# Performance work log

Measured on AMD Instinct MI355X. Metric: run time of the kernel, lower is better.

The kernel has to match this reference:

```python
import jax, jax.numpy as jnp
import numpy as np

EPS = 1e-5  # torch LayerNorm default


def _layernorm(x, g, b):
    mu = jnp.mean(x, axis=-1, keepdims=True)
    var = jnp.mean(jnp.square(x - mu), axis=-1, keepdims=True)
    return (x - mu) * jax.lax.rsqrt(var + EPS) * g + b


def _sparse_window_attn(x, wq, wk, wv, wo, span, stride, head_num):
    B, L, D = x.shape
    d = D // head_num  # dim_QK == dim_V == dim_q // head_num
    Q = (x @ wq.T).reshape(B, L, head_num, d).transpose(0, 2, 1, 3)  # [B,H,L,d]
    K = (x @ wk.T).reshape(B, L, head_num, d).transpose(0, 2, 1, 3)
    V = (x @ wv.T).reshape(B, L, head_num, d).transpose(0, 2, 1, 3)
    s = jnp.arange(span)
    i = jnp.arange(L)
    kvi = s[:, None] - (span - 1) + stride * i[None, :]       # [S,L] key index per (offset, query)
    valid = (kvi >= 0) & (kvi < L)
    kvic = jnp.clip(kvi, 0, L - 1)
    Kg = K[:, :, kvic, :]                                     # [B,H,S,L,d]
    scores = jnp.einsum('bhld,bhsld->bhsl', Q, Kg) / jnp.sqrt(jnp.float32(d))
    scores = jnp.where(valid[None, None], scores, -jnp.inf)
    p = jax.nn.softmax(scores, axis=2)                        # softmax over span (dim 2 in torch)
    Vg = V[:, :, kvic, :]                                     # [B,H,S,L,d]
    o = jnp.einsum('bhsl,bhsld->bhld', p, Vg)                 # invalid entries have p==0
    o = o.transpose(0, 2, 1, 3).reshape(B, L, D)
    return o @ wo.T


def setup_inputs() -> dict:
    key = jax.random.key(0)
    ks = jax.random.split(key, 8)
    B, L, D = 2, 2048, 512
    sc = 1.0 / np.sqrt(D)
    return {
        'query': jax.random.normal(ks[0], (B, L, D), jnp.float32),
        'ln_g': jnp.ones((D,), jnp.float32),
        'ln_b': jnp.zeros((D,), jnp.float32),
        'wq': jax.random.normal(ks[1], (D, D), jnp.float32) * sc,
        'wk': jax.random.normal(ks[2], (D, D), jnp.float32) * sc,
        'wv': jax.random.normal(ks[3], (D, D), jnp.float32) * sc,
        'wo': jax.random.normal(ks[4], (D, D), jnp.float32) * sc,
        'w1': jax.random.normal(ks[5], (2 * D, D), jnp.float32) * sc,
        'b1': jnp.zeros((2 * D,), jnp.float32),
        'w2': jax.random.normal(ks[6], (D, 2 * D), jnp.float32) * (1.0 / np.sqrt(2 * D)),
        'b2': jnp.zeros((D,), jnp.float32),
        'span': 64,
        'stride': 1,
        'head_num': 8,
    }


def reference(query, ln_g, ln_b, wq, wk, wv, wo, w1, b1, w2, b2, span, stride, head_num):
    # NOTE: the torch block applies the SAME LayerNorm (shared params) twice.
    x = _layernorm(query, ln_g, ln_b)
    x = _sparse_window_attn(x, wq, wk, wv, wo, span, stride, head_num)
    query = x + query
    x = _layernorm(query, ln_g, ln_b)
    x = jax.nn.gelu(x @ w1.T + b1, approximate=False) @ w2.T + b2
    return x + query
```

## Files before the change

### kernel.cpp

```cpp
#include <hip/hip_runtime.h>
#include <hip/hip_bf16.h>
#include <cmath>

typedef __bf16 bf16;
typedef __attribute__((ext_vector_type(8))) __bf16 bf16x8;
typedef __attribute__((ext_vector_type(4))) __bf16 bf16x4;
typedef __attribute__((ext_vector_type(4))) float f32x4;
typedef __attribute__((ext_vector_type(4))) unsigned int u32x4;

#define LD_B 2
#define LD_L 2048
#define LD_D 512
#define N_HEAD 8
#define HD 64
#define NTOK (LD_B * LD_L)
#define QKV_LD 1536

__device__ __forceinline__ void gload16(const void* g, void* l) {
  __builtin_amdgcn_global_load_lds(
      (const __attribute__((address_space(1))) void*)g,
      (__attribute__((address_space(3))) void*)l, 16, 0, 0);
}

__global__ __launch_bounds__(256) void prep_kernel(
    const float* __restrict__ x, const float* __restrict__ g,
    const float* __restrict__ b, bf16* __restrict__ xln,
    const float* __restrict__ s0, const float* __restrict__ s1,
    const float* __restrict__ s2, const float* __restrict__ s3,
    const float* __restrict__ s4, const float* __restrict__ s5,
    bf16* __restrict__ d0, bf16* __restrict__ d1, bf16* __restrict__ d2,
    bf16* __restrict__ d3, bf16* __restrict__ d4, bf16* __restrict__ d5)
{
  if (blockIdx.x >= 1024) {
    int idx = (blockIdx.x - 1024) * 256 + threadIdx.x;
    const float* src; bf16* dst; int off;
    if (idx < 262144) {
      int seg = idx >> 16; off = idx & 65535;
      src = seg == 0 ? s0 : seg == 1 ? s1 : seg == 2 ? s2 : s3;
      dst = seg == 0 ? d0 : seg == 1 ? d1 : seg == 2 ? d2 : d3;
    } else {
      int t = idx - 262144;
      int seg = t >> 17; off = t & 131071;
      src = seg ? s5 : s4;
      dst = seg ? d5 : d4;
    }
    f32x4 v = ((const f32x4*)src)[off];
    bf16x4 o;
    o[0] = (bf16)v[0]; o[1] = (bf16)v[1]; o[2] = (bf16)v[2]; o[3] = (bf16)v[3];
    ((bf16x4*)dst)[off] = o;
    return;
  }
  const int wid = threadIdx.x >> 6, lane = threadIdx.x & 63;
  const int row = blockIdx.x * 4 + wid;
  const f32x4* xr = (const f32x4*)(x + (size_t)row * LD_D);
  f32x4 v0 = xr[lane * 2], v1 = xr[lane * 2 + 1];
  float s = v0[0] + v0[1] + v0[2] + v0[3] + v1[0] + v1[1] + v1[2] + v1[3];
#pragma unroll
  for (int off = 32; off; off >>= 1) s += __shfl_xor(s, off);
  const float mu = s * (1.f / 512.f);
  float vs = 0.f;
#pragma unroll
  for (int i = 0; i < 4; ++i) {
    float a0 = v0[i] - mu; vs += a0 * a0;
    float a1 = v1[i] - mu; vs += a1 * a1;
  }
#pragma unroll
  for (int off = 32; off; off >>= 1) vs += __shfl_xor(vs, off);
  const float rstd = rsqrtf(vs * (1.f / 512.f) + 1e-5f);
  const f32x4* gr = (const f32x4*)g;
  const f32x4* br = (const f32x4*)b;
  f32x4 g0 = gr[lane * 2], g1 = gr[lane * 2 + 1];
  f32x4 b0 = br[lane * 2], b1 = br[lane * 2 + 1];
  bf16x8 o;
#pragma unroll
  for (int i = 0; i < 4; ++i) o[i] = (bf16)((v0[i] - mu) * rstd * g0[i] + b0[i]);
#pragma unroll
  for (int i = 0; i < 4; ++i) o[i + 4] = (bf16)((v1[i] - mu) * rstd * g1[i] + b1[i]);
  *(bf16x8*)(&xln[(size_t)row * LD_D + lane * 8]) = o;
}

__global__ __launch_bounds__(256) void ln_kernel(
    const float* __restrict__ x, const float* __restrict__ g,
    const float* __restrict__ b, bf16* __restrict__ out)
{
  const int wid = threadIdx.x >> 6, lane = threadIdx.x & 63;
  const int row = blockIdx.x * 4 + wid;
  const f32x4* xr = (const f32x4*)(x + (size_t)row * LD_D);
  f32x4 v0 = xr[lane * 2], v1 = xr[lane * 2 + 1];
  float s = v0[0] + v0[1] + v0[2] + v0[3] + v1[0] + v1[1] + v1[2] + v1[3];
#pragma unroll
  for (int off = 32; off; off >>= 1) s += __shfl_xor(s, off);
  const float mu = s * (1.f / 512.f);
  float vs = 0.f;
#pragma unroll
  for (int i = 0; i < 4; ++i) {
    float a0 = v0[i] - mu; vs += a0 * a0;
    float a1 = v1[i] - mu; vs += a1 * a1;
  }
#pragma unroll
  for (int off = 32; off; off >>= 1) vs += __shfl_xor(vs, off);
  const float rstd = rsqrtf(vs * (1.f / 512.f) + 1e-5f);
  const f32x4* gr = (const f32x4*)g;
  const f32x4* br = (const f32x4*)b;
  f32x4 g0 = gr[lane * 2], g1 = gr[lane * 2 + 1];
  f32x4 b0 = br[lane * 2], b1 = br[lane * 2 + 1];
  bf16x8 o;
#pragma unroll
  for (int i = 0; i < 4; ++i) o[i] = (bf16)((v0[i] - mu) * rstd * g0[i] + b0[i]);
#pragma unroll
  for (int i = 0; i < 4; ++i) o[i + 4] = (bf16)((v1[i] - mu) * rstd * g1[i] + b1[i]);
  *(bf16x8*)(&out[(size_t)row * LD_D + lane * 8]) = o;
}

template <int EPI>
__global__ __launch_bounds__(256) void gemm_kernel(
    const bf16* __restrict__ A, const bf16* __restrict__ Bw,
    int M, int N, int K, bf16* __restrict__ Cb, float* __restrict__ Cf,
    const float* __restrict__ bias, const float* __restrict__ res)
{
  __shared__ bf16 As[2][4096];
  __shared__ bf16 Bs[2][4096];
  const int tid = threadIdx.x;
  const int lane = tid & 63, wid = tid >> 6;
  const int wm = wid >> 1, wn = wid & 1;
  const int l15 = lane & 15, kg = lane >> 4;
  const int row0 = blockIdx.x * 64, col0 = blockIdx.y * 64;

  int srow[2], scol[2];
#pragma unroll
  for (int i = 0; i < 2; ++i) {
    int c = i * 256 + tid;
    srow[i] = c >> 3;
    scol[i] = ((c & 7) ^ (srow[i] & 7)) * 8;
  }

  f32x4 acc[2][2];
#pragma unroll
  for (int m = 0; m < 2; ++m)
#pragma unroll
    for (int n = 0; n < 2; ++n) acc[m][n] = (f32x4){0.f, 0.f, 0.f, 0.f};

  const int nt = K >> 6;
#define STAGE(buf, k0)                                                      \
  {                                                                         \
    _Pragma("unroll")                                                       \
    for (int i = 0; i < 2; ++i) {                                           \
      const bf16* ga = A + (size_t)(row0 + srow[i]) * K + (k0) + scol[i];   \
      const bf16* gb = Bw + (size_t)(col0 + srow[i]) * K + (k0) + scol[i];  \
      char* la = (char*)&As[buf][0] + (i * 4 + wid) * 1024;                 \
      char* lb = (char*)&Bs[buf][0] + (i * 4 + wid) * 1024;                 \
      gload16(ga, la);                                                      \
      gload16(gb, lb);                                                      \
    }                                                                       \
  }

  STAGE(0, 0);
  __syncthreads();
  for (int t = 0; t < nt; ++t) {
    if (t + 1 < nt) STAGE((t + 1) & 1, (t + 1) << 6);
    const char* pa = (const char*)&As[t & 1][0];
    const char* pb = (const char*)&Bs[t & 1][0];
#pragma unroll
    for (int kk = 0; kk < 2; ++kk) {
      bf16x8 af[2], bf[2];
#pragma unroll
      for (int m = 0; m < 2; ++m) {
        const int r = wm * 32 + m * 16 + l15;
        int off = r * 128 + kk * 64 + kg * 16;
        off ^= (r & 7) << 4;
        af[m] = *(const bf16x8*)(pa + off);
      }
#pragma unroll
      for (int n = 0; n < 2; ++n) {
        const int r = wn * 32 + n * 16 + l15;
        int off = r * 128 + kk * 64 + kg * 16;
        off ^= (r & 7) << 4;
        bf[n] = *(const bf16x8*)(pb + off);
      }
#pragma unroll
      for (int m = 0; m < 2; ++m)
#pragma unroll
        for (int n = 0; n < 2; ++n)
          acc[m][n] = __builtin_amdgcn_mfma_f32_16x16x32_bf16(af[m], bf[n], acc[m][n], 0, 0, 0);
    }
    __syncthreads();
  }
#undef STAGE

  const int orow = row0 + wm * 32, ocol = col0 + wn * 32;
#pragma unroll
  for (int m = 0; m < 2; ++m) {
#pragma unroll
    for (int n = 0; n < 2; ++n) {
#pragma unroll
      for (int e = 0; e < 4; ++e) {
        const int rr = orow + m * 16 + kg * 4 + e;
        const int cc = ocol + n * 16 + l15;
        const float v = acc[m][n][e];
        const size_t oi = (size_t)rr * N + cc;
        if constexpr (EPI == 0) {
          Cb[oi] = (bf16)v;
        } else if constexpr (EPI == 1) {
          Cf[oi] = v + res[oi];
        } else if constexpr (EPI == 2) {
          float t2 = v + bias[cc];
          Cb[oi] = (bf16)(0.5f * t2 * (1.f + erff(t2 * 0.70710678118654752f)));
        } else {
          Cf[oi] = v + bias[cc] + res[oi];
        }
      }
    }
  }
}

__global__ __launch_bounds__(256) void attn_kernel(
    const bf16* __restrict__ QKV, bf16* __restrict__ Og)
{
  constexpr int STK = 72;
  constexpr int STP = 136;
  __shared__ bf16 Ks[128][STK];
  __shared__ bf16 Qs[64][STK];
  __shared__ bf16 Vt[64][STP];
  __shared__ bf16 Ps[4][16][STP];
  const int tid = threadIdx.x;
  const int qt = blockIdx.x, bh = blockIdx.y;
  const int b = bh >> 3, h = bh & 7;
  const int q0 = qt * 64;
  const int j0 = q0 - 63;
  const size_t baseQ = (size_t)b * LD_L * QKV_LD + h * HD;
  const size_t baseK = baseQ + 512;
  const size_t baseV = baseQ + 1024;
  const size_t baseO = (size_t)b * LD_L * LD_D + h * HD;

  for (int c = tid; c < 128 * 8; c += 256) {
    const int r = c >> 3, d0 = (c & 7) * 8;
    const int j = j0 + r;
    u32x4 kv = (u32x4){0u, 0u, 0u, 0u};
    bf16x8 vv = (bf16x8)(__bf16)0.f;
    if (j >= 0 && j < LD_L) {
      kv = *(const u32x4*)(QKV + baseK + (size_t)j * QKV_LD + d0);
      vv = *(const bf16x8*)(QKV + baseV + (size_t)j * QKV_LD + d0);
    }
    *(u32x4*)(&Ks[r][d0]) = kv;
#pragma unroll
    for (int dd = 0; dd < 8; ++dd) Vt[d0 + dd][r] = vv[dd];
  }
  for (int c = tid; c < 64 * 8; c += 256) {
    const int r = c >> 3, d0 = (c & 7) * 8;
    *(u32x4*)(&Qs[r][d0]) =
        *(const u32x4*)(QKV + baseQ + (size_t)(q0 + r) * QKV_LD + d0);
  }
  __syncthreads();

  const int lane = tid & 63, wid = tid >> 6;
  const int l15 = lane & 15, kg = lane >> 4;
  const int klo = 63 - q0;

  bf16x8 qf[2];
#pragma unroll
  for (int kk = 0; kk < 2; ++kk)
    qf[kk] = *(const bf16x8*)(&Qs[wid * 16 + l15][kk * 32 + kg * 8]);
  f32x4 s[8];
#pragma unroll
  for (int n = 0; n < 8; ++n) s[n] = (f32x4){0.f, 0.f, 0.f, 0.f};
#pragma unroll
  for (int kk = 0; kk < 2; ++kk)
#pragma unroll
    for (int n = 0; n < 8; ++n) {
      bf16x8 kf = *(const bf16x8*)(&Ks[n * 16 + l15][kk * 32 + kg * 8]);
      s[n] = __builtin_amdgcn_mfma_f32_16x16x32_bf16(qf[kk], kf, s[n], 0, 0, 0);
    }

  float p[8][4];
  float mx[4], sm[4];
#pragma unroll
  for (int e = 0; e < 4; ++e) { mx[e] = -INFINITY; sm[e] = 0.f; }
#pragma unroll
  for (int n = 0; n < 8; ++n) {
    const int k = n * 16 + l15;
#pragma unroll
    for (int e = 0; e < 4; ++e) {
      const int qi = wid * 16 + kg * 4 + e;
      const bool ok = (k >= qi) & (k <= qi + 63) & (k >= klo);
      float sv = ok ? s[n][e] * 0.125f : -INFINITY;
      p[n][e] = sv;
      mx[e] = fmaxf(mx[e], sv);
    }
  }
#pragma unroll
  for (int off = 8; off; off >>= 1)
#pragma unroll
    for (int e = 0; e < 4; ++e) mx[e] = fmaxf(mx[e], __shfl_xor(mx[e], off));
#pragma unroll
  for (int n = 0; n < 8; ++n)
#pragma unroll
    for (int e = 0; e < 4; ++e) {
      float pv = (p[n][e] == -INFINITY) ? 0.f : __expf(p[n][e] - mx[e]);
      p[n][e] = pv;
      sm[e] += pv;
    }
#pragma unroll
  for (int off = 8; off; off >>= 1)
#pragma unroll
    for (int e = 0; e < 4; ++e) sm[e] += __shfl_xor(sm[e], off);
  float rs[4];
#pragma unroll
  for (int e = 0; e < 4; ++e) rs[e] = 1.f / sm[e];

#pragma unroll
  for (int n = 0; n < 8; ++n)
#pragma unroll
    for (int e = 0; e < 4; ++e)
      Ps[wid][kg * 4 + e][n * 16 + l15] = (bf16)(p[n][e] * rs[e]);

  f32x4 o[4];
#pragma unroll
  for (int n = 0; n < 4; ++n) o[n] = (f32x4){0.f, 0.f, 0.f, 0.f};
#pragma unroll
  for (int ks = 0; ks < 4; ++ks) {
    bf16x8 pf = *(const bf16x8*)(&Ps[wid][l15][ks * 32 + kg * 8]);
#pragma unroll
    for (int n = 0; n < 4; ++n) {
      bf16x8 vf = *(const bf16x8*)(&Vt[n * 16 + l15][ks * 32 + kg * 8]);
      o[n] = __builtin_amdgcn_mfma_f32_16x16x32_bf16(pf, vf, o[n], 0, 0, 0);
    }
  }

  const int q = q0 + wid * 16 + kg * 4;
#pragma unroll
  for (int n = 0; n < 4; ++n)
#pragma unroll
    for (int e = 0; e < 4; ++e)
      Og[baseO + (size_t)(q + e) * LD_D + n * 16 + l15] = (bf16)o[n][e];
}

extern "C" void kernel_launch(void* const* d_in, const int* in_sizes, int n_in,
                              void* d_out, int out_size, void* d_ws, size_t ws_size,
                              hipStream_t stream)
{
  const float* query = (const float*)d_in[0];
  const float* ln_g = (const float*)d_in[1];
  const float* ln_b = (const float*)d_in[2];
  const float* wq = (const float*)d_in[3];
  const float* wk = (const float*)d_in[4];
  const float* wv = (const float*)d_in[5];
  const float* wo = (const float*)d_in[6];
  const float* w1 = (const float*)d_in[7];
  const float* b1 = (const float*)d_in[8];
  const float* w2 = (const float*)d_in[9];
  const float* b2 = (const float*)d_in[10];
  float* out = (float*)d_out;

  char* ws = (char*)d_ws;
  bf16* WQKVb = (bf16*)(ws + 0x000000);
  bf16* WOb = (bf16*)(ws + 0x180000);
  bf16* W1b = (bf16*)(ws + 0x200000);
  bf16* W2b = (bf16*)(ws + 0x300000);
  bf16* XLN = (bf16*)(ws + 0x400000);
  bf16* QKVb = (bf16*)(ws + 0x800000);
  bf16* ATb = (bf16*)(ws + 0x1400000);
  float* Q2 = (float*)(ws + 0x1800000);
  bf16* YLN = (bf16*)(ws + 0x2000000);
  bf16* Hb = (bf16*)(ws + 0x2400000);

  prep_kernel<<<3072, 256, 0, stream>>>(
      query, ln_g, ln_b, XLN,
      wq, wk, wv, wo, w1, w2,
      WQKVb, WQKVb + 262144, WQKVb + 524288, WOb, W1b, W2b);
  gemm_kernel<0><<<dim3(64, 24), 256, 0, stream>>>(
      XLN, WQKVb, NTOK, QKV_LD, 512, QKVb, nullptr, nullptr, nullptr);
  attn_kernel<<<dim3(32, 16), 256, 0, stream>>>(QKVb, ATb);
  gemm_kernel<1><<<dim3(64, 8), 256, 0, stream>>>(
      ATb, WOb, NTOK, 512, 512, nullptr, Q2, nullptr, query);
  ln_kernel<<<1024, 256, 0, stream>>>(Q2, ln_g, ln_b, YLN);
  gemm_kernel<2><<<dim3(64, 16), 256, 0, stream>>>(
      YLN, W1b, NTOK, 1024, 512, Hb, nullptr, b1, nullptr);
  gemm_kernel<3><<<dim3(64, 8), 256, 0, stream>>>(
      Hb, W2b, NTOK, 512, 1024, nullptr, out, b2, Q2);
}
```

Before: 149.8 us.

## Fuse all stages into one persistent cooperative kernel with grid syncs

Replaces the seven separate kernel launches (prep, QKV GEMM, attention, out-proj GEMM, LN, FFN1, FFN2) with a single persistent cooperative kernel. Each stage loops over tiles with a grid-stride loop, and stages are separated by grid.sync(). Shared memory is now one shared byte buffer carved up per stage. This removes launch gaps and per-kernel tail effects. In exchange it caps the grid at 512 blocks, adds grid-wide barrier costs, and limits occupancy, since all stages must share one register and LDS budget.

```diff
diff --git a/kernel.cpp b/kernel.cpp
--- a/kernel.cpp
+++ b/kernel.cpp
@@ -1,6 +1,9 @@
 #include <hip/hip_runtime.h>
 #include <hip/hip_bf16.h>
+#include <hip/hip_cooperative_groups.h>
 #include <cmath>
+
+namespace cg = cooperative_groups;
 
 typedef __bf16 bf16;
 typedef __attribute__((ext_vector_type(8))) __bf16 bf16x8;
@@ -11,10 +14,11 @@
 #define LD_B 2
 #define LD_L 2048
 #define LD_D 512
-#define N_HEAD 8
 #define HD 64
 #define NTOK (LD_B * LD_L)
 #define QKV_LD 1536
+
+#define SMEM_BYTES 62464
 
 __device__ __forceinline__ void gload16(const void* g, void* l) {
   __builtin_amdgcn_global_load_lds(
@@ -22,36 +26,10 @@
       (__attribute__((address_space(3))) void*)l, 16, 0, 0);
 }
 
-__global__ __launch_bounds__(256) void prep_kernel(
+__device__ __forceinline__ void ln_row(
     const float* __restrict__ x, const float* __restrict__ g,
-    const float* __restrict__ b, bf16* __restrict__ xln,
-    const float* __restrict__ s0, const float* __restrict__ s1,
-    const float* __restrict__ s2, const float* __restrict__ s3,
-    const float* __restrict__ s4, const float* __restrict__ s5,
-    bf16* __restrict__ d0, bf16* __restrict__ d1, bf16* __restrict__ d2,
-    bf16* __restrict__ d3, bf16* __restrict__ d4, bf16* __restrict__ d5)
-{
-  if (blockIdx.x >= 1024) {
-    int idx = (blockIdx.x - 1024) * 256 + threadIdx.x;
-    const float* src; bf16* dst; int off;
-    if (idx < 262144) {
-      int seg = idx >> 16; off = idx & 65535;
-      src = seg == 0 ? s0 : seg == 1 ? s1 : seg == 2 ? s2 : s3;
-      dst = seg == 0 ? d0 : seg == 1 ? d1 : seg == 2 ? d2 : d3;
-    } else {
-      int t = idx - 262144;
-      int seg = t >> 17; off = t & 131071;
-      src = seg ? s5 : s4;
-      dst = seg ? d5 : d4;
-    }
-    f32x4 v = ((const f32x4*)src)[off];
-    bf16x4 o;
-    o[0] = (bf16)v[0]; o[1] = (bf16)v[1]; o[2] = (bf16)v[2]; o[3] = (bf16)v[3];
-    ((bf16x4*)dst)[off] = o;
-    return;
-  }
-  const int wid = threadIdx.x >> 6, lane = threadIdx.x & 63;
-  const int row = blockIdx.x * 4 + wid;
+    const float* __restrict__ b, bf16* __restrict__ out, int row, int lane)
+{
   const f32x4* xr = (const f32x4*)(x + (size_t)row * LD_D);
   f32x4 v0 = xr[lane * 2], v1 = xr[lane * 2 + 1];
   float s = v0[0] + v0[1] + v0[2] + v0[3] + v1[0] + v1[1] + v1[2] + v1[3];
@@ -76,63 +54,24 @@
   for (int i = 0; i < 4; ++i) o[i] = (bf16)((v0[i] - mu) * rstd * g0[i] + b0[i]);
 #pragma unroll
   for (int i = 0; i < 4; ++i) o[i + 4] = (bf16)((v1[i] - mu) * rstd * g1[i] + b1[i]);
-  *(bf16x8*)(&xln[(size_t)row * LD_D + lane * 8]) = o;
-}
-
-__global__ __launch_bounds__(256) void ln_kernel(
-    const float* __restrict__ x, const float* __restrict__ g,
-    const float* __restrict__ b, bf16* __restrict__ out)
-{
-  const int wid = threadIdx.x >> 6, lane = threadIdx.x & 63;
-  const int row = blockIdx.x * 4 + wid;
-  const f32x4* xr = (const f32x4*)(x + (size_t)row * LD_D);
-  f32x4 v0 = xr[lane * 2], v1 = xr[lane * 2 + 1];
-  float s = v0[0] + v0[1] + v0[2] + v0[3] + v1[0] + v1[1] + v1[2] + v1[3];
-#pragma unroll
-  for (int off = 32; off; off >>= 1) s += __shfl_xor(s, off);
-  const float mu = s * (1.f / 512.f);
-  float vs = 0.f;
-#pragma unroll
-  for (int i = 0; i < 4; ++i) {
-    float a0 = v0[i] - mu; vs += a0 * a0;
-    float a1 = v1[i] - mu; vs += a1 * a1;
-  }
-#pragma unroll
-  for (int off = 32; off; off >>= 1) vs += __shfl_xor(vs, off);
-  const float rstd = rsqrtf(vs * (1.f / 512.f) + 1e-5f);
-  const f32x4* gr = (const f32x4*)g;
-  const f32x4* br = (const f32x4*)b;
-  f32x4 g0 = gr[lane * 2], g1 = gr[lane * 2 + 1];
-  f32x4 b0 = br[lane * 2], b1 = br[lane * 2 + 1];
-  bf16x8 o;
-#pragma unroll
-  for (int i = 0; i < 4; ++i) o[i] = (bf16)((v0[i] - mu) * rstd * g0[i] + b0[i]);
-#pragma unroll
-  for (int i = 0; i < 4; ++i) o[i + 4] = (bf16)((v1[i] - mu) * rstd * g1[i] + b1[i]);
   *(bf16x8*)(&out[(size_t)row * LD_D + lane * 8]) = o;
 }
 
 template <int EPI>
-__global__ __launch_bounds__(256) void gemm_kernel(
+__device__ __forceinline__ void gemm_tile(
     const bf16* __restrict__ A, const bf16* __restrict__ Bw,
-    int M, int N, int K, bf16* __restrict__ Cb, float* __restrict__ Cf,
-    const float* __restrict__ bias, const float* __restrict__ res)
-{
-  __shared__ bf16 As[2][4096];
-  __shared__ bf16 Bs[2][4096];
+    int N, int K, bf16* __restrict__ Cb, float* __restrict__ Cf,
+    const float* __restrict__ bias, const float* __restrict__ res,
+    int row0, int col0, char* __restrict__ smem)
+{
   const int tid = threadIdx.x;
   const int lane = tid & 63, wid = tid >> 6;
   const int wm = wid >> 1, wn = wid & 1;
   const int l15 = lane & 15, kg = lane >> 4;
-  const int row0 = blockIdx.x * 64, col0 = blockIdx.y * 64;
-
-  int srow[2], scol[2];
-#pragma unroll
-  for (int i = 0; i < 2; ++i) {
-    int c = i * 256 + tid;
-    srow[i] = c >> 3;
-    scol[i] = ((c & 7) ^ (srow[i] & 7)) * 8;
-  }
+
+  const int c0 = tid, c1 = 256 + tid;
+  const int srow0 = c0 >> 3, scol0 = ((c0 & 7) ^ (srow0 & 7)) * 8;
+  const int srow1 = c1 >> 3, scol1 = ((c1 & 7) ^ (srow1 & 7)) * 8;
 
   f32x4 acc[2][2];
 #pragma unroll
@@ -141,25 +80,22 @@
     for (int n = 0; n < 2; ++n) acc[m][n] = (f32x4){0.f, 0.f, 0.f, 0.f};
 
   const int nt = K >> 6;
-#define STAGE(buf, k0)                                                      \
-  {                                                                         \
-    _Pragma("unroll")                                                       \
-    for (int i = 0; i < 2; ++i) {                                           \
-      const bf16* ga = A + (size_t)(row0 + srow[i]) * K + (k0) + scol[i];   \
-      const bf16* gb = Bw + (size_t)(col0 + srow[i]) * K + (k0) + scol[i];  \
-      char* la = (char*)&As[buf][0] + (i * 4 + wid) * 1024;                 \
-      char* lb = (char*)&Bs[buf][0] + (i * 4 + wid) * 1024;                 \
-      gload16(ga, la);                                                      \
-      gload16(gb, lb);                                                      \
-    }                                                                       \
+#define STAGE(buf, k0)                                                        \
+  {                                                                           \
+    char* baseA = smem + (buf) * 8192;                                        \
+    char* baseB = smem + 16384 + (buf) * 8192;                                \
+    gload16(A + (size_t)(row0 + srow0) * K + (k0) + scol0, baseA + wid * 1024);\
+    gload16(A + (size_t)(row0 + srow1) * K + (k0) + scol1, baseA + 4096 + wid * 1024);\
+    gload16(Bw + (size_t)(col0 + srow0) * K + (k0) + scol0, baseB + wid * 1024);\
+    gload16(Bw + (size_t)(col0 + srow1) * K + (k0) + scol1, baseB + 4096 + wid * 1024);\
   }
 
   STAGE(0, 0);
   __syncthreads();
   for (int t = 0; t < nt; ++t) {
     if (t + 1 < nt) STAGE((t + 1) & 1, (t + 1) << 6);
-    const char* pa = (const char*)&As[t & 1][0];
-    const char* pb = (const char*)&Bs[t & 1][0];
+    const char* pa = smem + (t & 1) * 8192;
+    const char* pb = smem + 16384 + (t & 1) * 8192;
 #pragma unroll
     for (int kk = 0; kk < 2; ++kk) {
       bf16x8 af[2], bf[2];
@@ -213,17 +149,15 @@
   }
 }
 
-__global__ __launch_bounds__(256) void attn_kernel(
-    const bf16* __restrict__ QKV, bf16* __restrict__ Og)
-{
-  constexpr int STK = 72;
-  constexpr int STP = 136;
-  __shared__ bf16 Ks[128][STK];
-  __shared__ bf16 Qs[64][STK];
-  __shared__ bf16 Vt[64][STP];
-  __shared__ bf16 Ps[4][16][STP];
+__device__ __forceinline__ void attn_tile(
+    const bf16* __restrict__ QKV, bf16* __restrict__ Og,
+    int qt, int bh, char* __restrict__ smem)
+{
+  bf16 (*Ks)[72]  = (bf16(*)[72])(smem);
+  bf16 (*Qs)[72]  = (bf16(*)[72])(smem + 18432);
+  bf16 (*Vt)[136] = (bf16(*)[136])(smem + 27648);
+  bf16 (*Ps)[136] = (bf16(*)[136])(smem + 45056);
   const int tid = threadIdx.x;
-  const int qt = blockIdx.x, bh = blockIdx.y;
   const int b = bh >> 3, h = bh & 7;
   const int q0 = qt * 64;
   const int j0 = q0 - 63;
@@ -232,6 +166,7 @@
   const size_t baseV = baseQ + 1024;
   const size_t baseO = (size_t)b * LD_L * LD_D + h * HD;
 
+  __syncthreads();
   for (int c = tid; c < 128 * 8; c += 256) {
     const int r = c >> 3, d0 = (c & 7) * 8;
     const int j = j0 + r;
@@ -311,14 +246,14 @@
   for (int n = 0; n < 8; ++n)
 #pragma unroll
     for (int e = 0; e < 4; ++e)
-      Ps[wid][kg * 4 + e][n * 16 + l15] = (bf16)(p[n][e] * rs[e]);
+      Ps[wid * 16 + kg * 4 + e][n * 16 + l15] = (bf16)(p[n][e] * rs[e]);
 
   f32x4 o[4];
 #pragma unroll
   for (int n = 0; n < 4; ++n) o[n] = (f32x4){0.f, 0.f, 0.f, 0.f};
 #pragma unroll
   for (int ks = 0; ks < 4; ++ks) {
-    bf16x8 pf = *(const bf16x8*)(&Ps[wid][l15][ks * 32 + kg * 8]);
+    bf16x8 pf = *(const bf16x8*)(&Ps[wid * 16 + l15][ks * 32 + kg * 8]);
 #pragma unroll
     for (int n = 0; n < 4; ++n) {
       bf16x8 vf = *(const bf16x8*)(&Vt[n * 16 + l15][ks * 32 + kg * 8]);
@@ -332,6 +267,77 @@
 #pragma unroll
     for (int e = 0; e < 4; ++e)
       Og[baseO + (size_t)(q + e) * LD_D + n * 16 + l15] = (bf16)o[n][e];
+}
+
+__global__ __launch_bounds__(256, 2) void fused_block_kernel(
+    const float* __restrict__ query, const float* __restrict__ ln_g,
+    const float* __restrict__ ln_b,
+    const float* __restrict__ wq, const float* __restrict__ wk,
+    const float* __restrict__ wv, const float* __restrict__ wo,
+    const float* __restrict__ w1, const float* __restrict__ b1,
+    const float* __restrict__ w2, const float* __restrict__ b2,
+    float* __restrict__ out,
+    bf16* __restrict__ WQKVb, bf16* __restrict__ WOb,
+    bf16* __restrict__ W1b, bf16* __restrict__ W2b,
+    bf16* __restrict__ XLN, bf16* __restrict__ QKVb,
+    bf16* __restrict__ ATb, float* __restrict__ Q2,
+    bf16* __restrict__ YLN, bf16* __restrict__ Hb)
+{
+  __shared__ __align__(16) char smem[SMEM_BYTES];
+  cg::grid_group grid = cg::this_grid();
+  const int tid = threadIdx.x;
+  const int wi = blockIdx.x;
+  const int G = gridDim.x;
+  const int lane = tid & 63, wid = tid >> 6;
+
+  for (int idx = wi * 256 + tid; idx < 524288; idx += G * 256) {
+    const float* src; bf16* dst; int off;
+    if (idx < 262144) {
+      int seg = idx >> 16; off = idx & 65535;
+      src = seg == 0 ? wq : seg == 1 ? wk : seg == 2 ? wv : wo;
+      dst = seg == 0 ? WQKVb : seg == 1 ? (WQKVb + 262144)
+          : seg == 2 ? (WQKVb + 524288) : WOb;
+    } else {
+      int t = idx - 262144;
+      int seg = t >> 17; off = t & 131071;
+      src = seg ? w2 : w1;
+      dst = seg ? W2b : W1b;
+    }
+    f32x4 v = ((const f32x4*)src)[off];
+    bf16x4 o;
+    o[0] = (bf16)v[0]; o[1] = (bf16)v[1]; o[2] = (bf16)v[2]; o[3] = (bf16)v[3];
+    ((bf16x4*)dst)[off] = o;
+  }
+  for (int row = wi * 4 + wid; row < NTOK; row += G * 4)
+    ln_row(query, ln_g, ln_b, XLN, row, lane);
+  grid.sync();
+
+  for (int t = wi; t < 1536; t += G)
+    gemm_tile<0>(XLN, WQKVb, QKV_LD, 512, QKVb, nullptr, nullptr, nullptr,
+                 (t & 63) << 6, (t >> 6) << 6, smem);
+  grid.sync();
+
+  for (int it = wi; it < 512; it += G)
+    attn_tile(QKVb, ATb, it & 31, it >> 5, smem);
+  grid.sync();
+
+  for (int t = wi; t < 512; t += G)
+    gemm_tile<1>(ATb, WOb, 512, 512, nullptr, Q2, nullptr, query,
+                 (t & 63) << 6, (t >> 6) << 6, smem);
+  grid.sync();
+
+  for (int row = wi * 4 + wid; row < NTOK; row += G * 4)
+    ln_row(Q2, ln_g, ln_b, YLN, row, lane);
+  grid.sync();
+
+  for (int t = wi; t < 1024; t += G)
+    gemm_tile<2>(YLN, W1b, 1024, 512, Hb, nullptr, b1, nullptr,
+                 (t & 63) << 6, (t >> 6) << 6, smem);
+  grid.sync();
+
+  for (int t = wi; t < 512; t += G)
+    gemm_tile<3>(Hb, W2b, 512, 1024, nullptr, out, b2, Q2,
+                 (t & 63) << 6, (t >> 6) << 6, smem);
 }
 
 extern "C" void kernel_launch(void* const* d_in, const int* in_sizes, int n_in,
@@ -363,18 +369,21 @@
   bf16* YLN = (bf16*)(ws + 0x2000000);
   bf16* Hb = (bf16*)(ws + 0x2400000);
 
-  prep_kernel<<<3072, 256, 0, stream>>>(
-      query, ln_g, ln_b, XLN,
-      wq, wk, wv, wo, w1, w2,
-      WQKVb, WQKVb + 262144, WQKVb + 524288, WOb, W1b, W2b);
-  gemm_kernel<0><<<dim3(64, 24), 256, 0, stream>>>(
-      XLN, WQKVb, NTOK, QKV_LD, 512, QKVb, nullptr, nullptr, nullptr);
-  attn_kernel<<<dim3(32, 16), 256, 0, stream>>>(QKVb, ATb);
-  gemm_kernel<1><<<dim3(64, 8), 256, 0, stream>>>(
-      ATb, WOb, NTOK, 512, 512, nullptr, Q2, nullptr, query);
-  ln_kernel<<<1024, 256, 0, stream>>>(Q2, ln_g, ln_b, YLN);
-  gemm_kernel<2><<<dim3(64, 16), 256, 0, stream>>>(
-      YLN, W1b, NTOK, 1024, 512, Hb, nullptr, b1, nullptr);
-  gemm_kernel<3><<<dim3(64, 8), 256, 0, stream>>>(
-      Hb, W2b, NTOK, 512, 1024, nullptr, out, b2, Q2);
-}
+  int nb = 0;
+  if (hipOccupancyMaxActiveBlocksPerMultiprocessor(&nb, fused_block_kernel, 256, 0)
+          != hipSuccess || nb < 1)
+    nb = 1;
+  int grid = nb * 256;
+  if (grid > 512) grid = 512;
+
+  void* args[] = {
+      (void*)&query, (void*)&ln_g, (void*)&ln_b,
+      (void*)&wq, (void*)&wk, (void*)&wv, (void*)&wo,
+      (void*)&w1, (void*)&b1, (void*)&w2, (void*)&b2,
+      (void*)&out,
+      (void*)&WQKVb, (void*)&WOb, (void*)&W1b, (void*)&W2b,
+      (void*)&XLN, (void*)&QKVb, (void*)&ATb, (void*)&Q2,
+      (void*)&YLN, (void*)&Hb};
+  hipLaunchCooperativeKernel((void*)fused_block_kernel, dim3(grid), dim3(256),
+                             args, 0, stream);
+}
```

After: 379.6 us. 153% more time.

## Rework GEMMs into triple-buffered ring with compile-time K and fine waits

Applied to the files above, without the earlier changes.

Replaces the double-buffered 64-wide K tile GEMM with a triple-buffered ring of 32-wide K steps. K is now a template constant, so the loop fully unrolls. Explicit vmcnt waits and raw s_barrier keep two prefetches in flight instead of doing a full __syncthreads per tile. The LDS swizzle is redone for the 64-byte row layout. This aims to hide global load latency in these small-grid GEMMs, at the cost of more barriers per K and a larger unrolled code size.

```diff
diff --git a/kernel.cpp b/kernel.cpp
--- a/kernel.cpp
+++ b/kernel.cpp
@@ -11,7 +11,6 @@
 #define LD_B 2
 #define LD_L 2048
 #define LD_D 512
-#define N_HEAD 8
 #define HD 64
 #define NTOK (LD_B * LD_L)
 #define QKV_LD 1536
@@ -112,26 +111,32 @@
   *(bf16x8*)(&out[(size_t)row * LD_D + lane * 8]) = o;
 }
 
-template <int EPI>
-__global__ __launch_bounds__(256) void gemm_kernel(
-    const bf16* __restrict__ A, const bf16* __restrict__ Bw,
-    int M, int N, int K, bf16* __restrict__ Cb, float* __restrict__ Cf,
+template <int K, int EPI>
+__device__ __forceinline__ void gemm_ring(
+    const bf16* __restrict__ A, const bf16* __restrict__ Bw,
+    int N, bf16* __restrict__ Cb, float* __restrict__ Cf,
     const float* __restrict__ bias, const float* __restrict__ res)
 {
-  __shared__ bf16 As[2][4096];
-  __shared__ bf16 Bs[2][4096];
+  constexpr int NSTEP = K / 32;
+  __shared__ bf16 As[3][2048];
+  __shared__ bf16 Bs[3][2048];
   const int tid = threadIdx.x;
   const int lane = tid & 63, wid = tid >> 6;
   const int wm = wid >> 1, wn = wid & 1;
   const int l15 = lane & 15, kg = lane >> 4;
   const int row0 = blockIdx.x * 64, col0 = blockIdx.y * 64;
 
-  int srow[2], scol[2];
-#pragma unroll
-  for (int i = 0; i < 2; ++i) {
-    int c = i * 256 + tid;
-    srow[i] = c >> 3;
-    scol[i] = ((c & 7) ^ (srow[i] & 7)) * 8;
+  const int srow = tid >> 2;
+  const int scol = ((tid & 3) ^ ((srow >> 1) & 3)) * 8;
+  const bf16* gA = A + (size_t)(row0 + srow) * K + scol;
+  const bf16* gB = Bw + (size_t)(col0 + srow) * K + scol;
+  char* const lA = (char*)&As[0][0] + wid * 1024;
+  char* const lB = (char*)&Bs[0][0] + wid * 1024;
+
+#define STG(buf, kstep)                      \
+  {                                          \
+    gload16(gA + (kstep) * 32, lA + (buf) * 4096); \
+    gload16(gB + (kstep) * 32, lB + (buf) * 4096); \
   }
 
   f32x4 acc[2][2];
@@ -140,52 +145,43 @@
 #pragma unroll
     for (int n = 0; n < 2; ++n) acc[m][n] = (f32x4){0.f, 0.f, 0.f, 0.f};
 
-  const int nt = K >> 6;
-#define STAGE(buf, k0)                                                      \
-  {                                                                         \
-    _Pragma("unroll")                                                       \
-    for (int i = 0; i < 2; ++i) {                                           \
-      const bf16* ga = A + (size_t)(row0 + srow[i]) * K + (k0) + scol[i];   \
-      const bf16* gb = Bw + (size_t)(col0 + srow[i]) * K + (k0) + scol[i];  \
-      char* la = (char*)&As[buf][0] + (i * 4 + wid) * 1024;                 \
-      char* lb = (char*)&Bs[buf][0] + (i * 4 + wid) * 1024;                 \
-      gload16(ga, la);                                                      \
-      gload16(gb, lb);                                                      \
-    }                                                                       \
-  }
-
-  STAGE(0, 0);
-  __syncthreads();
-  for (int t = 0; t < nt; ++t) {
-    if (t + 1 < nt) STAGE((t + 1) & 1, (t + 1) << 6);
-    const char* pa = (const char*)&As[t & 1][0];
-    const char* pb = (const char*)&Bs[t & 1][0];
-#pragma unroll
-    for (int kk = 0; kk < 2; ++kk) {
-      bf16x8 af[2], bf[2];
-#pragma unroll
-      for (int m = 0; m < 2; ++m) {
-        const int r = wm * 32 + m * 16 + l15;
-        int off = r * 128 + kk * 64 + kg * 16;
-        off ^= (r & 7) << 4;
-        af[m] = *(const bf16x8*)(pa + off);
-      }
-#pragma unroll
-      for (int n = 0; n < 2; ++n) {
-        const int r = wn * 32 + n * 16 + l15;
-        int off = r * 128 + kk * 64 + kg * 16;
-        off ^= (r & 7) << 4;
-        bf[n] = *(const bf16x8*)(pb + off);
-      }
-#pragma unroll
-      for (int m = 0; m < 2; ++m)
-#pragma unroll
-        for (int n = 0; n < 2; ++n)
-          acc[m][n] = __builtin_amdgcn_mfma_f32_16x16x32_bf16(af[m], bf[n], acc[m][n], 0, 0, 0);
-    }
-    __syncthreads();
-  }
-#undef STAGE
+  STG(0, 0);
+  STG(1, 1);
+  asm volatile("s_waitcnt vmcnt(2)" ::: "memory");
+  __builtin_amdgcn_s_barrier();
+  __builtin_amdgcn_sched_barrier(0);
+
+#pragma unroll
+  for (int t = 0; t < NSTEP; ++t) {
+    if (t + 2 < NSTEP) STG((t + 2) % 3, t + 2);
+    const char* pa = (const char*)&As[t % 3][0];
+    const char* pb = (const char*)&Bs[t % 3][0];
+    bf16x8 af[2], bf[2];
+#pragma unroll
+    for (int m = 0; m < 2; ++m) {
+      const int r = wm * 32 + m * 16 + l15;
+      af[m] = *(const bf16x8*)(pa + r * 64 + ((kg ^ ((r >> 1) & 3)) << 4));
+    }
+#pragma unroll
+    for (int n = 0; n < 2; ++n) {
+      const int r = wn * 32 + n * 16 + l15;
+      bf[n] = *(const bf16x8*)(pb + r * 64 + ((kg ^ ((r >> 1) & 3)) << 4));
+    }
+#pragma unroll
+    for (int m = 0; m < 2; ++m)
+#pragma unroll
+      for (int n = 0; n < 2; ++n)
+        acc[m][n] = __builtin_amdgcn_mfma_f32_16x16x32_bf16(af[m], bf[n], acc[m][n], 0, 0, 0);
+    if (t + 1 < NSTEP) {
+      if (t + 2 < NSTEP)
+        asm volatile("s_waitcnt vmcnt(2)" ::: "memory");
+      else
+        asm volatile("s_waitcnt vmcnt(0)" ::: "memory");
+      __builtin_amdgcn_s_barrier();
+      __builtin_amdgcn_sched_barrier(0);
+    }
+  }
+#undef STG
 
   const int orow = row0 + wm * 32, ocol = col0 + wn * 32;
 #pragma unroll
@@ -213,6 +209,32 @@
   }
 }
 
+__global__ __launch_bounds__(256) void gemm_qkv(
+    const bf16* __restrict__ A, const bf16* __restrict__ Bw,
+    bf16* __restrict__ Cb)
+{
+  gemm_ring<512, 0>(A, Bw, QKV_LD, Cb, nullptr, nullptr, nullptr);
+}
+__global__ __launch_bounds__(256) void gemm_oproj(
+    const bf16* __restrict__ A, const bf16* __restrict__ Bw,
+    float* __restrict__ Cf, const float* __restrict__ res)
+{
+  gemm_ring<512, 1>(A, Bw, 512, nullptr, Cf, nullptr, res);
+}
+__global__ __launch_bounds__(256) void gemm_mlp1(
+    const bf16* __restrict__ A, const bf16* __restrict__ Bw,
+    bf16* __restrict__ Cb, const float* __restrict__ bias)
+{
+  gemm_ring<512, 2>(A, Bw, 1024, Cb, nullptr, bias, nullptr);
+}
+__global__ __launch_bounds__(256) void gemm_mlp2(
+    const bf16* __restrict__ A, const bf16* __restrict__ Bw,
+    float* __restrict__ Cf, const float* __restrict__ bias,
+    const float* __restrict__ res)
+{
+  gemm_ring<1024, 3>(A, Bw, 512, nullptr, Cf, bias, res);
+}
+
 __global__ __launch_bounds__(256) void attn_kernel(
     const bf16* __restrict__ QKV, bf16* __restrict__ Og)
 {
@@ -367,14 +389,10 @@
       query, ln_g, ln_b, XLN,
       wq, wk, wv, wo, w1, w2,
       WQKVb, WQKVb + 262144, WQKVb + 524288, WOb, W1b, W2b);
-  gemm_kernel<0><<<dim3(64, 24), 256, 0, stream>>>(
-      XLN, WQKVb, NTOK, QKV_LD, 512, QKVb, nullptr, nullptr, nullptr);
+  gemm_qkv<<<dim3(64, 24), 256, 0, stream>>>(XLN, WQKVb, QKVb);
   attn_kernel<<<dim3(32, 16), 256, 0, stream>>>(QKVb, ATb);
-  gemm_kernel<1><<<dim3(64, 8), 256, 0, stream>>>(
-      ATb, WOb, NTOK, 512, 512, nullptr, Q2, nullptr, query);
+  gemm_oproj<<<dim3(64, 8), 256, 0, stream>>>(ATb, WOb, Q2, query);
   ln_kernel<<<1024, 256, 0, stream>>>(Q2, ln_g, ln_b, YLN);
-  gemm_kernel<2><<<dim3(64, 16), 256, 0, stream>>>(
-      YLN, W1b, NTOK, 1024, 512, Hb, nullptr, b1, nullptr);
-  gemm_kernel<3><<<dim3(64, 8), 256, 0, stream>>>(
-      Hb, W2b, NTOK, 512, 1024, nullptr, out, b2, Q2);
-}
+  gemm_mlp1<<<dim3(64, 16), 256, 0, stream>>>(YLN, W1b, Hb, b1);
+  gemm_mlp2<<<dim3(64, 8), 256, 0, stream>>>(Hb, W2b, out, b2, Q2);
+}
```

Result: slower. 153.2 us (+2.3%).
